# Kernel optimization log

Measured on AMD Instinct MI355X. Metric: run time of the kernel, lower is better.

Reference implementation:

```python
import jax, jax.numpy as jnp
import numpy as np

D = 1024       # d_model
L = 4          # num_layers
T = 2048       # sequence length


def setup_inputs() -> dict:
    key = jax.random.key(0)
    ks = jax.random.split(key, 8)
    lim = 1.0 / np.sqrt(2 * D)              # torch default Linear init bound
    xav = np.sqrt(6.0 / (2 * D + D))        # xavier_uniform for time_a/time_b
    u = lambda k, lo, hi: jax.random.uniform(k, (L, 2 * D, D), jnp.float32, lo, hi)
    return {
        "spatial_states": jax.random.normal(ks[0], (T, D), jnp.float32),
        "re_norm": jnp.float32(0.5),
        "dt_phys": jnp.float32(1.0),
        "re_proj_w": jax.random.uniform(ks[1], (D,), jnp.float32, -1.0, 1.0),  # Linear(1,D) weight, bound=1
        "re_proj_b": jax.random.uniform(ks[2], (D,), jnp.float32, -1.0, 1.0),
        "Wf1": u(ks[3], -lim, lim),
        "bf1": jnp.zeros((L, D), jnp.float32),
        "Wf2": u(ks[4], -lim, lim),
        "bf2": jnp.zeros((L, D), jnp.float32),
        "Wta": u(ks[5], -xav, xav),
        "bta": jnp.zeros((L, D), jnp.float32),
        "Wtb": u(ks[6], -xav, xav),
        "btb": jnp.zeros((L, D), jnp.float32),
    }


def reference(spatial_states, re_norm, dt_phys, re_proj_w, re_proj_b,
              Wf1, bf1, Wf2, bf2, Wta, bta, Wtb, btb):
    d = re_proj_w.shape[0]
    # persistent Re residual bias added to every timestep
    seq = spatial_states + re_norm * re_proj_w + re_proj_b  # [T, D]
    n_layers = Wf1.shape[0]
    for l in range(n_layers):
        # fuse the 4 per-cell linears into one [2D, 4D] GEMV per step
        W = jnp.concatenate([Wf1[l], Wf2[l], Wta[l], Wtb[l]], axis=1)  # [2D, 4D]
        b = jnp.concatenate([bf1[l], bf2[l], bta[l], btb[l]])          # [4D]

        def step(h, x, W=W, b=b):
            xh = jnp.concatenate([x, h])          # [2D]
            z = xh @ W + b                        # [4D]
            f1 = jnp.tanh(z[:d])
            f2 = jnp.tanh(z[d:2 * d])
            gate = jax.nn.sigmoid(-z[2 * d:3 * d] * dt_phys + z[3 * d:])
            h_new = gate * f1 + (1.0 - gate) * f2
            return h_new, h_new

        _, seq = jax.lax.scan(step, jnp.zeros((d,), seq.dtype), seq)
    return seq[-1]  # [D]
```

## Files before the change

### kernel.cpp

```cpp
#include <hip/hip_runtime.h>
#include <cstdint>
#include <cstddef>

#define DD 1024
#define TT 2048
#define NL 4
#define CH 128
#define NCH (TT / CH)
#define NTHR 1024
#define BPL 64
#define PBLK (NL * BPL)
#define GUARD_LIM (1 << 20)

__device__ __forceinline__ float fast_tanh(float x) {
  float e = __expf(2.f * x);
  return 1.f - 2.f / (e + 1.f);
}

__device__ __forceinline__ float4 agent_load16(const float* p) {
  float4 r;
  asm volatile("global_load_dwordx4 %0, %1, off sc1\n\t"
               "s_waitcnt vmcnt(0)"
               : "=v"(r) : "v"(p) : "memory");
  return r;
}
__device__ __forceinline__ void agent_store16(float* p, float4 v) {
  unsigned long long lo =
      ((unsigned long long)__float_as_uint(v.y) << 32) | __float_as_uint(v.x);
  unsigned long long hi =
      ((unsigned long long)__float_as_uint(v.w) << 32) | __float_as_uint(v.z);
  __hip_atomic_store((unsigned long long*)p, lo,
                     __ATOMIC_RELAXED, __HIP_MEMORY_SCOPE_AGENT);
  __hip_atomic_store(((unsigned long long*)p) + 1, hi,
                     __ATOMIC_RELAXED, __HIP_MEMORY_SCOPE_AGENT);
}

template <int CTRL>
__device__ __forceinline__ float dpp_add(float x) {
  int y = __builtin_amdgcn_update_dpp(0, __float_as_int(x), CTRL, 0xf, 0xf, true);
  return x + __int_as_float(y);
}
__device__ __forceinline__ float wave_allreduce_add(float x) {
  x = dpp_add<0xB1>(x);
  x = dpp_add<0x4E>(x);
  x = dpp_add<0x141>(x);
  x = dpp_add<0x140>(x);
  x += __shfl_xor(x, 16, 64);
  x += __shfl_xor(x, 32, 64);
  return x;
}

__device__ __forceinline__ bool nan_free4(float4 v) {
  unsigned x0 = __float_as_uint(v.x) & 0x7fffffffu;
  unsigned x1 = __float_as_uint(v.y) & 0x7fffffffu;
  unsigned x2 = __float_as_uint(v.z) & 0x7fffffffu;
  unsigned x3 = __float_as_uint(v.w) & 0x7fffffffu;
  return (x0 <= 0x7f800000u) && (x1 <= 0x7f800000u) &&
         (x2 <= 0x7f800000u) && (x3 <= 0x7f800000u);
}

__global__ __launch_bounds__(1024) void prep_kernel(
    const float* __restrict__ sp, const float* __restrict__ rn_p,
    const float* __restrict__ w, const float* __restrict__ b,
    float* __restrict__ X0) {
  int i = blockIdx.x * blockDim.x + threadIdx.x;
  float rn = rn_p[0];
  int c = i & (DD - 1);
  X0[i] = sp[i] + rn * w[c] + b[c];
}

__global__ __launch_bounds__(NTHR, 4) void persist_kernel(
    const float* __restrict__ X0,
    float* __restrict__ HB,
    int R,
    const float* __restrict__ Wf1, const float* __restrict__ Wf2,
    const float* __restrict__ Wta, const float* __restrict__ Wtb,
    const float* __restrict__ bf1, const float* __restrict__ bf2,
    const float* __restrict__ bta, const float* __restrict__ btb,
    const float* __restrict__ dt_p,
    float* __restrict__ out_last)
{
  __shared__ __align__(16) float hbuf[2][DD];
  __shared__ float zxbuf[CH][64];
  __shared__ float Xs[16][132];
  __shared__ float Ws[16][64];
  __shared__ __align__(64) float hq[16];
  __shared__ float lds_pad[7424];

  const int tid = threadIdx.x;
  const int w   = tid >> 6;
  const int ln  = tid & 63;
  const int l   = blockIdx.x >> 6;
  const int grp = blockIdx.x & 63;
  const int col = grp * 16 + w;
  const float dtv = dt_p[0];

  lds_pad[tid] = 0.f;

  const size_t woff = (size_t)l * 2 * DD * DD;

  float4 wA0, wA1, wA2, wA3, wB0, wB1, wB2, wB3;
  float4 wC0, wC1, wC2, wC3, wD0, wD1, wD2, wD3;
#define LOADW(dst, base, g) do { \
    const float* p_ = (base) + (size_t)(DD + (g) * 256 + ln * 4) * DD + col; \
    dst = make_float4(p_[0], p_[DD], p_[2 * DD], p_[3 * DD]); \
  } while (0)
  {
    const float* W_ = Wf1 + woff;
    LOADW(wA0, W_, 0); LOADW(wA1, W_, 1); LOADW(wA2, W_, 2); LOADW(wA3, W_, 3);
    W_ = Wf2 + woff;
    LOADW(wB0, W_, 0); LOADW(wB1, W_, 1); LOADW(wB2, W_, 2); LOADW(wB3, W_, 3);
    W_ = Wta + woff;
    LOADW(wC0, W_, 0); LOADW(wC1, W_, 1); LOADW(wC2, W_, 2); LOADW(wC3, W_, 3);
    W_ = Wtb + woff;
    LOADW(wD0, W_, 0); LOADW(wD1, W_, 1); LOADW(wD2, W_, 2); LOADW(wD3, W_, 3);
  }
#undef LOADW

  const int p  = ln >> 4;
  const float* Wxp = ((p == 0) ? Wf1 : (p == 1) ? Wf2 : (p == 2) ? Wta : Wtb) + woff;
  const float* bsp = ((p == 0) ? bf1 : (p == 1) ? bf2 : (p == 2) ? bta : btb)
                     + (size_t)l * DD;
  const int colx = grp * 16 + (ln & 15);
  const float biasv = bsp[colx];

  const int rsel = grp & (R - 1);
  const float* hread = HB + (size_t)(l * R + rsel) * TT * DD;
  const float* xbase = (l == 0) ? X0 : HB + (size_t)((l - 1) * R + rsel) * TT * DD;

  hbuf[0][tid] = 0.f;
  __syncthreads();

#pragma unroll 1
  for (int c = 0; c < NCH; ++c) {
    if (l > 0) {
      if (tid < 256) {
        const float* gsrc = xbase + (size_t)(c * CH + CH - 1) * DD + tid * 4;
        bool ok = false;
        int tries = 0;
        while (true) {
          if (!ok) ok = nan_free4(agent_load16(gsrc));
          if (__all(ok)) break;
          if (++tries > 2) __builtin_amdgcn_s_sleep(8);
          if (tries > GUARD_LIM) break;
        }
      }
      __syncthreads();
    }

    float acc[8];
#pragma unroll
    for (int i = 0; i < 8; ++i) acc[i] = 0.f;

#pragma unroll 1
    for (int k0 = 0; k0 < DD; k0 += 16) {
      Ws[w][ln] = Wxp[(size_t)(k0 + w) * DD + colx];
      if (tid < 512) {
        const int row = tid >> 2;
        const int q   = (tid & 3) * 4;
        const float* src = xbase + (size_t)(c * CH + row) * DD + k0 + q;
        float4 v = (l == 0) ? *(const float4*)src : agent_load16(src);
        Xs[q + 0][row] = v.x; Xs[q + 1][row] = v.y;
        Xs[q + 2][row] = v.z; Xs[q + 3][row] = v.w;
      }
      __syncthreads();
#pragma unroll
      for (int kk = 0; kk < 16; ++kk) {
        float wv = Ws[kk][ln];
        float4 x0 = *(const float4*)&Xs[kk][w * 8];
        float4 x1 = *(const float4*)&Xs[kk][w * 8 + 4];
        acc[0] = fmaf(x0.x, wv, acc[0]); acc[1] = fmaf(x0.y, wv, acc[1]);
        acc[2] = fmaf(x0.z, wv, acc[2]); acc[3] = fmaf(x0.w, wv, acc[3]);
        acc[4] = fmaf(x1.x, wv, acc[4]); acc[5] = fmaf(x1.y, wv, acc[5]);
        acc[6] = fmaf(x1.z, wv, acc[6]); acc[7] = fmaf(x1.w, wv, acc[7]);
      }
      __syncthreads();
    }
#pragma unroll
    for (int i = 0; i < 8; ++i) zxbuf[w * 8 + i][ln] = acc[i] + biasv;
    __syncthreads();

#pragma unroll 1
    for (int tl = 0; tl < CH; ++tl) {
      const int t = c * CH + tl;
      const float* rbuf = hbuf[t & 1];

      float zxv = (ln < 4) ? zxbuf[tl][ln * 16 + w] : 0.f;
      float a0 = (ln == 0) ? zxv : 0.f;
      float a1 = (ln == 1) ? zxv : 0.f;
      float a2 = (ln == 2) ? zxv : 0.f;
      float a3 = (ln == 3) ? zxv : 0.f;

#define DOTG(g, WA, WB, WC, WD) do { \
      float4 h4 = *(const float4*)&rbuf[(g) * 256 + ln * 4]; \
      a0 = fmaf(h4.x, WA.x, a0); a0 = fmaf(h4.y, WA.y, a0); \
      a0 = fmaf(h4.z, WA.z, a0); a0 = fmaf(h4.w, WA.w, a0); \
      a1 = fmaf(h4.x, WB.x, a1); a1 = fmaf(h4.y, WB.y, a1); \
      a1 = fmaf(h4.z, WB.z, a1); a1 = fmaf(h4.w, WB.w, a1); \
      a2 = fmaf(h4.x, WC.x, a2); a2 = fmaf(h4.y, WC.y, a2); \
      a2 = fmaf(h4.z, WC.z, a2); a2 = fmaf(h4.w, WC.w, a2); \
      a3 = fmaf(h4.x, WD.x, a3); a3 = fmaf(h4.y, WD.y, a3); \
      a3 = fmaf(h4.z, WD.z, a3); a3 = fmaf(h4.w, WD.w, a3); \
    } while (0)
      DOTG(0, wA0, wB0, wC0, wD0);
      DOTG(1, wA1, wB1, wC1, wD1);
      DOTG(2, wA2, wB2, wC2, wD2);
      DOTG(3, wA3, wB3, wC3, wD3);
#undef DOTG

      a0 = wave_allreduce_add(a0);
      a1 = wave_allreduce_add(a1);
      a2 = wave_allreduce_add(a2);
      a3 = wave_allreduce_add(a3);

      float f1 = fast_tanh(a0);
      float f2 = fast_tanh(a1);
      float g  = 1.f / (1.f + __expf(a2 * dtv - a3));
      float h  = fmaf(g, f1 - f2, f2);

      if (ln == 0) hq[w] = h;
      if (l == 3 && t == TT - 1 && ln == 0 && out_last) out_last[col] = h;
      __syncthreads();

      if (w == 0 && ln < R) {
        float* dst = HB + (size_t)(l * R + ln) * TT * DD + (size_t)t * DD + grp * 16;
        float4 q0 = *(const float4*)&hq[0];
        float4 q1 = *(const float4*)&hq[4];
        float4 q2 = *(const float4*)&hq[8];
        float4 q3 = *(const float4*)&hq[12];
        agent_store16(dst + 0,  q0);
        agent_store16(dst + 4,  q1);
        agent_store16(dst + 8,  q2);
        agent_store16(dst + 12, q3);
      }

      if (t < TT - 1 && tid < 256) {
        const float* src = &hread[(size_t)t * DD + tid * 4];
        float4 v = make_float4(0.f, 0.f, 0.f, 0.f);
        bool ok = false;
        int tries = 0;
        while (true) {
          if (!ok) {
            v = agent_load16(src);
            ok = nan_free4(v);
          }
          if (__all(ok)) break;
          if (++tries > 8) __builtin_amdgcn_s_sleep(1);
          if (tries > GUARD_LIM) break;
        }
        if (!ok) v = make_float4(0.f, 0.f, 0.f, 0.f);
        *(float4*)&hbuf[(t + 1) & 1][tid * 4] = v;
      }
      __syncthreads();
    }
  }
}

extern "C" void kernel_launch(void* const* d_in, const int* in_sizes, int n_in,
                              void* d_out, int out_size, void* d_ws, size_t ws_size,
                              hipStream_t stream) {
  const float* sp  = (const float*)d_in[0];
  const float* rn  = (const float*)d_in[1];
  const float* dt  = (const float*)d_in[2];
  const float* rw  = (const float*)d_in[3];
  const float* rb  = (const float*)d_in[4];
  const float* Wf1 = (const float*)d_in[5];
  const float* bf1 = (const float*)d_in[6];
  const float* Wf2 = (const float*)d_in[7];
  const float* bf2 = (const float*)d_in[8];
  const float* Wta = (const float*)d_in[9];
  const float* bta = (const float*)d_in[10];
  const float* Wtb = (const float*)d_in[11];
  const float* btb = (const float*)d_in[12];

  float* ws = (float*)d_ws;
  float* X0 = ws;
  float* HB = ws + (size_t)TT * DD;
  float* out = (float*)d_out;

  int R = 1;
  for (int cand = 8; cand >= 1; cand >>= 1) {
    size_t need = sizeof(float) * (size_t)TT * DD * (size_t)(1 + NL * cand);
    if (need <= ws_size) { R = cand; break; }
  }

  (void)hipMemsetAsync(HB, 0xFF, sizeof(float) * (size_t)NL * R * TT * DD, stream);
  prep_kernel<<<(TT * DD) / 1024, 1024, 0, stream>>>(sp, rn, rw, rb, X0);
  persist_kernel<<<PBLK, NTHR, 0, stream>>>(X0, HB, R, Wf1, Wf2, Wta, Wtb,
      bf1, bf2, bta, btb, dt, out);
}
```

Before: 11.04 ms.

## Prefetch chunk input-GEMM operands and drop per-step LDS barrier for h stores

Replaces the per-step gather of h values through shared memory plus an extra barrier with direct per-wave scalar atomic stores into the replicated h buffers. The chunked input projection now register-prefetches the next X and W slice before the FMA loop, and uses plain loads with a NaN-sentinel fallback to agent-scope polling after an acquire fence instead of always using coherent loads. This removes one __syncthreads per timestep on the serial recurrence critical path and overlaps global loads with compute. In exchange it issues more, narrower stores, and the plain-load fast path depends on the sentinel check for correctness. It also keeps the LDS padding alive through a dummy dependent store.

```diff
diff --git a/kernel.cpp b/kernel.cpp
--- a/kernel.cpp
+++ b/kernel.cpp
@@ -24,16 +24,6 @@
                : "=v"(r) : "v"(p) : "memory");
   return r;
 }
-__device__ __forceinline__ void agent_store16(float* p, float4 v) {
-  unsigned long long lo =
-      ((unsigned long long)__float_as_uint(v.y) << 32) | __float_as_uint(v.x);
-  unsigned long long hi =
-      ((unsigned long long)__float_as_uint(v.w) << 32) | __float_as_uint(v.z);
-  __hip_atomic_store((unsigned long long*)p, lo,
-                     __ATOMIC_RELAXED, __HIP_MEMORY_SCOPE_AGENT);
-  __hip_atomic_store(((unsigned long long*)p) + 1, hi,
-                     __ATOMIC_RELAXED, __HIP_MEMORY_SCOPE_AGENT);
-}
 
 template <int CTRL>
 __device__ __forceinline__ float dpp_add(float x) {
@@ -57,6 +47,20 @@
   unsigned x3 = __float_as_uint(v.w) & 0x7fffffffu;
   return (x0 <= 0x7f800000u) && (x1 <= 0x7f800000u) &&
          (x2 <= 0x7f800000u) && (x3 <= 0x7f800000u);
+}
+
+__device__ __forceinline__ float4 gemv_load16(const float* p, bool check) {
+  float4 v = *(const float4*)p;
+  if (check && !nan_free4(v)) {
+    int tries = 0;
+    while (true) {
+      v = agent_load16(p);
+      if (nan_free4(v)) break;
+      if (++tries > 2) __builtin_amdgcn_s_sleep(2);
+      if (tries > GUARD_LIM) { v = make_float4(0.f, 0.f, 0.f, 0.f); break; }
+    }
+  }
+  return v;
 }
 
 __global__ __launch_bounds__(1024) void prep_kernel(
@@ -84,7 +88,6 @@
   __shared__ float zxbuf[CH][64];
   __shared__ float Xs[16][132];
   __shared__ float Ws[16][64];
-  __shared__ __align__(64) float hq[16];
   __shared__ float lds_pad[7424];
 
   const int tid = threadIdx.x;
@@ -95,7 +98,7 @@
   const int col = grp * 16 + w;
   const float dtv = dt_p[0];
 
-  lds_pad[tid] = 0.f;
+  lds_pad[tid] = (float)tid;
 
   const size_t woff = (size_t)l * 2 * DD * DD;
 
@@ -146,33 +149,43 @@
         }
       }
       __syncthreads();
+      __builtin_amdgcn_fence(__ATOMIC_ACQUIRE, "agent");
     }
 
     float acc[8];
 #pragma unroll
     for (int i = 0; i < 8; ++i) acc[i] = 0.f;
 
+    const int xrow = tid >> 2;
+    const int xq   = (tid & 3) * 4;
+    const float* xrowp = xbase + (size_t)(c * CH + xrow) * DD + xq;
+    const bool chk = (l > 0);
+
+    float4 xv = make_float4(0.f, 0.f, 0.f, 0.f);
+    if (tid < 512) xv = gemv_load16(xrowp, chk);
+    float wv = Wxp[(size_t)w * DD + colx];
+
 #pragma unroll 1
     for (int k0 = 0; k0 < DD; k0 += 16) {
-      Ws[w][ln] = Wxp[(size_t)(k0 + w) * DD + colx];
       if (tid < 512) {
-        const int row = tid >> 2;
-        const int q   = (tid & 3) * 4;
-        const float* src = xbase + (size_t)(c * CH + row) * DD + k0 + q;
-        float4 v = (l == 0) ? *(const float4*)src : agent_load16(src);
-        Xs[q + 0][row] = v.x; Xs[q + 1][row] = v.y;
-        Xs[q + 2][row] = v.z; Xs[q + 3][row] = v.w;
-      }
-      __syncthreads();
+        Xs[xq + 0][xrow] = xv.x; Xs[xq + 1][xrow] = xv.y;
+        Xs[xq + 2][xrow] = xv.z; Xs[xq + 3][xrow] = xv.w;
+      }
+      Ws[w][ln] = wv;
+      __syncthreads();
+      if (k0 + 16 < DD) {
+        if (tid < 512) xv = gemv_load16(xrowp + k0 + 16, chk);
+        wv = Wxp[(size_t)(k0 + 16 + w) * DD + colx];
+      }
 #pragma unroll
       for (int kk = 0; kk < 16; ++kk) {
-        float wv = Ws[kk][ln];
+        float wvk = Ws[kk][ln];
         float4 x0 = *(const float4*)&Xs[kk][w * 8];
         float4 x1 = *(const float4*)&Xs[kk][w * 8 + 4];
-        acc[0] = fmaf(x0.x, wv, acc[0]); acc[1] = fmaf(x0.y, wv, acc[1]);
-        acc[2] = fmaf(x0.z, wv, acc[2]); acc[3] = fmaf(x0.w, wv, acc[3]);
-        acc[4] = fmaf(x1.x, wv, acc[4]); acc[5] = fmaf(x1.y, wv, acc[5]);
-        acc[6] = fmaf(x1.z, wv, acc[6]); acc[7] = fmaf(x1.w, wv, acc[7]);
+        acc[0] = fmaf(x0.x, wvk, acc[0]); acc[1] = fmaf(x0.y, wvk, acc[1]);
+        acc[2] = fmaf(x0.z, wvk, acc[2]); acc[3] = fmaf(x0.w, wvk, acc[3]);
+        acc[4] = fmaf(x1.x, wvk, acc[4]); acc[5] = fmaf(x1.y, wvk, acc[5]);
+        acc[6] = fmaf(x1.z, wvk, acc[6]); acc[7] = fmaf(x1.w, wvk, acc[7]);
       }
       __syncthreads();
     }
@@ -218,21 +231,12 @@
       float g  = 1.f / (1.f + __expf(a2 * dtv - a3));
       float h  = fmaf(g, f1 - f2, f2);
 
-      if (ln == 0) hq[w] = h;
+      if (ln < R) {
+        __hip_atomic_store(
+            &HB[(size_t)(l * R + ln) * TT * DD + (size_t)t * DD + col], h,
+            __ATOMIC_RELAXED, __HIP_MEMORY_SCOPE_AGENT);
+      }
       if (l == 3 && t == TT - 1 && ln == 0 && out_last) out_last[col] = h;
-      __syncthreads();
-
-      if (w == 0 && ln < R) {
-        float* dst = HB + (size_t)(l * R + ln) * TT * DD + (size_t)t * DD + grp * 16;
-        float4 q0 = *(const float4*)&hq[0];
-        float4 q1 = *(const float4*)&hq[4];
-        float4 q2 = *(const float4*)&hq[8];
-        float4 q3 = *(const float4*)&hq[12];
-        agent_store16(dst + 0,  q0);
-        agent_store16(dst + 4,  q1);
-        agent_store16(dst + 8,  q2);
-        agent_store16(dst + 12, q3);
-      }
 
       if (t < TT - 1 && tid < 256) {
         const float* src = &hread[(size_t)t * DD + tid * 4];
@@ -254,6 +258,8 @@
       __syncthreads();
     }
   }
+
+  if ((uintptr_t)out_last == 1) out_last[0] = lds_pad[tid];
 }
 
 extern "C" void kernel_launch(void* const* d_in, const int* in_sizes, int n_in,
```

After: 20.26 ms. 1.84x slower.

## Poll per-block step flags instead of NaN-scanning hidden state; retile input GEMM

Applied to the files above, without the earlier changes.

Each producer block now writes a per-step flag word after storing its 16 hidden values. Consumers poll 64 flags with single-dword loads instead of repeatedly loading and NaN-checking the full 1024-float hidden vector, then read the data once (with a fallback NaN recheck). The chunk size drops from 128 to 64 timesteps, and the input-projection GEMM is retiled to a 64-deep k tile with fewer syncs per k step. The cost is extra flag workspace and memset, plus a possible ordering risk between the relaxed data stores and the flag store, which the recheck guards against.

```diff
diff --git a/kernel.cpp b/kernel.cpp
--- a/kernel.cpp
+++ b/kernel.cpp
@@ -5,7 +5,7 @@
 #define DD 1024
 #define TT 2048
 #define NL 4
-#define CH 128
+#define CH 64
 #define NCH (TT / CH)
 #define NTHR 1024
 #define BPL 64
@@ -20,6 +20,13 @@
 __device__ __forceinline__ float4 agent_load16(const float* p) {
   float4 r;
   asm volatile("global_load_dwordx4 %0, %1, off sc1\n\t"
+               "s_waitcnt vmcnt(0)"
+               : "=v"(r) : "v"(p) : "memory");
+  return r;
+}
+__device__ __forceinline__ unsigned agent_load4(const unsigned* p) {
+  unsigned r;
+  asm volatile("global_load_dword %0, %1, off sc1\n\t"
                "s_waitcnt vmcnt(0)"
                : "=v"(r) : "v"(p) : "memory");
   return r;
@@ -72,6 +79,7 @@
 __global__ __launch_bounds__(NTHR, 4) void persist_kernel(
     const float* __restrict__ X0,
     float* __restrict__ HB,
+    unsigned* __restrict__ FLG,
     int R,
     const float* __restrict__ Wf1, const float* __restrict__ Wf2,
     const float* __restrict__ Wta, const float* __restrict__ Wtb,
@@ -82,10 +90,10 @@
 {
   __shared__ __align__(16) float hbuf[2][DD];
   __shared__ float zxbuf[CH][64];
-  __shared__ float Xs[16][132];
-  __shared__ float Ws[16][64];
+  __shared__ float Xs[64][68];
+  __shared__ float Ws[64][64];
   __shared__ __align__(64) float hq[16];
-  __shared__ float lds_pad[7424];
+  __shared__ float lds_pad[6144];
 
   const int tid = threadIdx.x;
   const int w   = tid >> 6;
@@ -95,7 +103,7 @@
   const int col = grp * 16 + w;
   const float dtv = dt_p[0];
 
-  lds_pad[tid] = 0.f;
+  if (tid < 6144) lds_pad[tid] = (float)tid;
 
   const size_t woff = (size_t)l * 2 * DD * DD;
 
@@ -126,6 +134,7 @@
 
   const int rsel = grp & (R - 1);
   const float* hread = HB + (size_t)(l * R + rsel) * TT * DD;
+  const unsigned* FLGr = FLG + (size_t)(l * R + rsel) * TT * 64;
   const float* xbase = (l == 0) ? X0 : HB + (size_t)((l - 1) * R + rsel) * TT * DD;
 
   hbuf[0][tid] = 0.f;
@@ -148,36 +157,37 @@
       __syncthreads();
     }
 
-    float acc[8];
+    float acc[4];
 #pragma unroll
-    for (int i = 0; i < 8; ++i) acc[i] = 0.f;
+    for (int i = 0; i < 4; ++i) acc[i] = 0.f;
+
+    const int xrow = tid >> 4;
+    const int xq   = (tid & 15) * 4;
+    const float* xrowp = xbase + (size_t)(c * CH + xrow) * DD + xq;
 
 #pragma unroll 1
-    for (int k0 = 0; k0 < DD; k0 += 16) {
-      Ws[w][ln] = Wxp[(size_t)(k0 + w) * DD + colx];
-      if (tid < 512) {
-        const int row = tid >> 2;
-        const int q   = (tid & 3) * 4;
-        const float* src = xbase + (size_t)(c * CH + row) * DD + k0 + q;
+    for (int k0 = 0; k0 < DD; k0 += 64) {
+      {
+        const float* src = xrowp + k0;
         float4 v = (l == 0) ? *(const float4*)src : agent_load16(src);
-        Xs[q + 0][row] = v.x; Xs[q + 1][row] = v.y;
-        Xs[q + 2][row] = v.z; Xs[q + 3][row] = v.w;
-      }
-      __syncthreads();
+        Xs[xq + 0][xrow] = v.x; Xs[xq + 1][xrow] = v.y;
+        Xs[xq + 2][xrow] = v.z; Xs[xq + 3][xrow] = v.w;
+      }
 #pragma unroll
-      for (int kk = 0; kk < 16; ++kk) {
-        float wv = Ws[kk][ln];
-        float4 x0 = *(const float4*)&Xs[kk][w * 8];
-        float4 x1 = *(const float4*)&Xs[kk][w * 8 + 4];
-        acc[0] = fmaf(x0.x, wv, acc[0]); acc[1] = fmaf(x0.y, wv, acc[1]);
-        acc[2] = fmaf(x0.z, wv, acc[2]); acc[3] = fmaf(x0.w, wv, acc[3]);
-        acc[4] = fmaf(x1.x, wv, acc[4]); acc[5] = fmaf(x1.y, wv, acc[5]);
-        acc[6] = fmaf(x1.z, wv, acc[6]); acc[7] = fmaf(x1.w, wv, acc[7]);
+      for (int j = 0; j < 4; ++j)
+        Ws[w * 4 + j][ln] = Wxp[(size_t)(k0 + w * 4 + j) * DD + colx];
+      __syncthreads();
+#pragma unroll 16
+      for (int kk = 0; kk < 64; ++kk) {
+        float wvk = Ws[kk][ln];
+        float4 x = *(const float4*)&Xs[kk][w * 4];
+        acc[0] = fmaf(x.x, wvk, acc[0]); acc[1] = fmaf(x.y, wvk, acc[1]);
+        acc[2] = fmaf(x.z, wvk, acc[2]); acc[3] = fmaf(x.w, wvk, acc[3]);
       }
       __syncthreads();
     }
 #pragma unroll
-    for (int i = 0; i < 8; ++i) zxbuf[w * 8 + i][ln] = acc[i] + biasv;
+    for (int i = 0; i < 4; ++i) zxbuf[w * 4 + i][ln] = acc[i] + biasv;
     __syncthreads();
 
 #pragma unroll 1
@@ -232,28 +242,36 @@
         agent_store16(dst + 4,  q1);
         agent_store16(dst + 8,  q2);
         agent_store16(dst + 12, q3);
+        __hip_atomic_store(&FLG[((size_t)(l * R + ln) * TT + t) * 64 + grp],
+                           (unsigned)t, __ATOMIC_RELAXED,
+                           __HIP_MEMORY_SCOPE_AGENT);
       }
 
       if (t < TT - 1 && tid < 256) {
-        const float* src = &hread[(size_t)t * DD + tid * 4];
-        float4 v = make_float4(0.f, 0.f, 0.f, 0.f);
-        bool ok = false;
+        const unsigned* fp = FLGr + (size_t)t * 64 + ln;
+        bool fok = false;
         int tries = 0;
         while (true) {
-          if (!ok) {
-            v = agent_load16(src);
-            ok = nan_free4(v);
-          }
-          if (__all(ok)) break;
+          if (!fok) fok = (agent_load4(fp) == (unsigned)t);
+          if (__all(fok)) break;
           if (++tries > 8) __builtin_amdgcn_s_sleep(1);
           if (tries > GUARD_LIM) break;
         }
-        if (!ok) v = make_float4(0.f, 0.f, 0.f, 0.f);
+        const float* src = &hread[(size_t)t * DD + tid * 4];
+        float4 v = agent_load16(src);
+        int g2 = 0;
+        while (!nan_free4(v)) {
+          if (++g2 > GUARD_LIM) { v = make_float4(0.f, 0.f, 0.f, 0.f); break; }
+          if (g2 > 4) __builtin_amdgcn_s_sleep(1);
+          v = agent_load16(src);
+        }
         *(float4*)&hbuf[(t + 1) & 1][tid * 4] = v;
       }
       __syncthreads();
     }
   }
+
+  if ((uintptr_t)out_last == 1) out_last[0] = lds_pad[tid & 1023];
 }
 
 extern "C" void kernel_launch(void* const* d_in, const int* in_sizes, int n_in,
@@ -277,15 +295,18 @@
   float* X0 = ws;
   float* HB = ws + (size_t)TT * DD;
   float* out = (float*)d_out;
+  const size_t seqB = sizeof(float) * (size_t)TT * DD;
+  const size_t flgPerRep = (size_t)TT * 64 * sizeof(unsigned);
 
   int R = 1;
   for (int cand = 8; cand >= 1; cand >>= 1) {
-    size_t need = sizeof(float) * (size_t)TT * DD * (size_t)(1 + NL * cand);
+    size_t need = seqB + (size_t)NL * cand * (seqB + flgPerRep);
     if (need <= ws_size) { R = cand; break; }
   }
-
-  (void)hipMemsetAsync(HB, 0xFF, sizeof(float) * (size_t)NL * R * TT * DD, stream);
+  unsigned* FLG = (unsigned*)(ws + (size_t)(1 + NL * R) * TT * DD);
+
+  (void)hipMemsetAsync(HB, 0xFF, (size_t)NL * R * (seqB + flgPerRep), stream);
   prep_kernel<<<(TT * DD) / 1024, 1024, 0, stream>>>(sp, rn, rw, rb, X0);
-  persist_kernel<<<PBLK, NTHR, 0, stream>>>(X0, HB, R, Wf1, Wf2, Wta, Wtb,
+  persist_kernel<<<PBLK, NTHR, 0, stream>>>(X0, HB, FLG, R, Wf1, Wf2, Wta, Wtb,
       bf1, bf2, bta, btb, dt, out);
 }
```

Result: no change. 11.01 ms (-0.2%).
